# Kernel optimization log

Measured on AMD Instinct MI355X. Metric: run time of the kernel, lower is better.

The kernel has to match this reference:

```python
import jax, jax.numpy as jnp
import numpy as np

NF4 = jnp.array([-1.0, -0.6961928009986877, -0.5250730514526367, -0.39491748809814453,
                 -0.28444138169288635, -0.18477343022823334, -0.09105003625154495, 0.0,
                 0.07958029955625534, 0.16093020141124725, 0.24611230194568634,
                 0.33791524171829224, 0.44070982933044434, 0.5626170039176941,
                 0.7229568362236023, 1.0], dtype=jnp.float32)

IN_FEATURES = 2048
OUT_FEATURES = 8192
BLOCK_SIZE = 64


def setup_inputs() -> dict:
    key = jax.random.key(0)
    k1, k2, k3, k4 = jax.random.split(key, 4)
    n_elems = OUT_FEATURES * IN_FEATURES
    n_blocks = n_elems // BLOCK_SIZE
    x = jax.random.normal(k1, (2, 2048, IN_FEATURES), dtype=jnp.float32)
    q = jax.random.randint(k2, (n_elems,), 0, 16, dtype=jnp.int32)
    scale = jax.random.uniform(k3, (n_blocks,), dtype=jnp.float32)  # absmax >= 0
    bias = jax.random.normal(k4, (OUT_FEATURES,), dtype=jnp.float32)
    return {"x": x, "q": q, "scale": scale, "bias": bias}


def reference(x, q, scale, bias):
    # Dequantize: NF4 table lookup per 4-bit code, per-block absmax scale.
    n_blocks = scale.shape[0]
    codes = q.reshape(n_blocks, BLOCK_SIZE)                  # (n_blocks, 64)
    w = NF4[codes] * scale[:, None]                          # (n_blocks, 64)
    w = w.reshape(OUT_FEATURES, IN_FEATURES)                 # (out, in)
    # F.linear: y = x @ W^T + b
    return jnp.einsum('bsi,oi->bso', x, w) + bias
```

## Files before the change

### kernel.cpp

```cpp
#include <hip/hip_runtime.h>
#include <stdint.h>

#define GM 4096
#define GN 8192
#define GK 2048

typedef float f32x4 __attribute__((ext_vector_type(4)));
typedef __bf16 bf16x8 __attribute__((ext_vector_type(8)));

__device__ __constant__ float NF4_LUT[16] = {
    -1.0f, -0.6961928009986877f, -0.5250730514526367f, -0.39491748809814453f,
    -0.28444138169288635f, -0.18477343022823334f, -0.09105003625154495f, 0.0f,
    0.07958029955625534f, 0.16093020141124725f, 0.24611230194568634f,
    0.33791524171829224f, 0.44070982933044434f, 0.5626170039176941f,
    0.7229568362236023f, 1.0f};

__device__ __forceinline__ unsigned short f32_to_bf16_rne(float f) {
  union { float f; uint32_t u; } v;
  v.f = f;
  uint32_t lsb = (v.u >> 16) & 1u;
  v.u += 0x7fffu + lsb;
  return (unsigned short)(v.u >> 16);
}

__global__ void __launch_bounds__(256) dequant_nf4_kernel(
    const int* __restrict__ q, const float* __restrict__ scale,
    unsigned short* __restrict__ w) {
  __shared__ float lut[16];
  if (threadIdx.x < 16) lut[threadIdx.x] = NF4_LUT[threadIdx.x];
  __syncthreads();
  int t = blockIdx.x * 256 + threadIdx.x;
  const int4* q4 = reinterpret_cast<const int4*>(q);
  int4 c0 = q4[2 * t];
  int4 c1 = q4[2 * t + 1];
  float s = scale[t >> 3];
  int codes[8] = {c0.x, c0.y, c0.z, c0.w, c1.x, c1.y, c1.z, c1.w};
  union { unsigned short u[8]; int4 v; } r;
#pragma unroll
  for (int j = 0; j < 8; ++j)
    r.u[j] = f32_to_bf16_rne(lut[codes[j] & 15] * s);
  reinterpret_cast<int4*>(w)[t] = r.v;
}

__global__ void __launch_bounds__(256) cvt_f32_bf16_kernel(
    const float* __restrict__ x, unsigned short* __restrict__ xb) {
  int t = blockIdx.x * 256 + threadIdx.x;
  const float4* x4 = reinterpret_cast<const float4*>(x);
  float4 a = x4[2 * t];
  float4 b = x4[2 * t + 1];
  union { unsigned short u[8]; int4 v; } r;
  r.u[0] = f32_to_bf16_rne(a.x); r.u[1] = f32_to_bf16_rne(a.y);
  r.u[2] = f32_to_bf16_rne(a.z); r.u[3] = f32_to_bf16_rne(a.w);
  r.u[4] = f32_to_bf16_rne(b.x); r.u[5] = f32_to_bf16_rne(b.y);
  r.u[6] = f32_to_bf16_rne(b.z); r.u[7] = f32_to_bf16_rne(b.w);
  reinterpret_cast<int4*>(xb)[t] = r.v;
}

#define AS1(p) ((const __attribute__((address_space(1))) void*)(p))
#define AS3(p) ((__attribute__((address_space(3))) void*)(p))
#define VM6() asm volatile("s_waitcnt vmcnt(6)" ::: "memory")
#define FENCE() asm volatile("" ::: "memory")
#define BAR() do { FENCE(); __builtin_amdgcn_s_barrier(); FENCE(); } while (0)

__global__ void __launch_bounds__(512, 2) gemm_8phase_kernel(
    const unsigned short* __restrict__ A,
    const unsigned short* __restrict__ B,
    const float* __restrict__ bias, float* __restrict__ C) {
  constexpr int BK = 64, NT = GK / BK;
  __shared__ __align__(16) unsigned short As[2 * 256 * 64];
  __shared__ __align__(16) unsigned short Bs[2 * 256 * 64];

  int bid = blockIdx.x;
  int swz = (bid & 7) * 64 + (bid >> 3);
  int brow = (swz >> 5) * 256;
  int bcol = (swz & 31) * 256;

  int tid = threadIdx.x;
  int lane = tid & 63;
  int wave = tid >> 6;
  int wr = wave >> 2;
  int wc = wave & 3;
  int fr = lane & 15;
  int slot = lane >> 4;
  int swc = (slot << 4) ^ ((fr & 7) << 4);

  const unsigned short* Abase = A + (size_t)brow * GK;
  const unsigned short* Bbase = B + (size_t)bcol * GK;

  int arow = (wr * 64 + fr) * 128;
  int brw = (wc * 32 + fr) * 128;

  f32x4 acc[8][4] = {};
  bf16x8 a0[2][4][2], a1[2][4][2], b0[2][2][2], b1[2][2][2];

  auto ldA = [&](int buf, int qm, int m, int kk) -> bf16x8 {
    int off = buf * 32768 + qm * 16384 + m * 2048 + arow + (swc ^ (kk << 6));
    return *reinterpret_cast<const bf16x8*>((const char*)As + off);
  };
  auto ldB = [&](int buf, int qn, int n, int kk) -> bf16x8 {
    int off = buf * 32768 + qn * 16384 + n * 2048 + brw + (swc ^ (kk << 6));
    return *reinterpret_cast<const bf16x8*>((const char*)Bs + off);
  };
  auto stage = [&](const unsigned short* gtile, unsigned short* lds, int buf,
                   int h, int kt) {
#pragma unroll
    for (int i = 0; i < 2; ++i) {
      int L = h * 16384 + i * 8192 + tid * 16;
      int s = L ^ (((L >> 7) & 7) << 4);
      __builtin_amdgcn_global_load_lds(
          AS1(gtile + (size_t)(s >> 7) * GK + kt + ((s & 127) >> 1)),
          AS3((char*)lds + buf * 32768 + L), 16, 0, 0);
    }
  };
  auto RD_A1 = [&](int p) {
#pragma unroll
    for (int m = 0; m < 4; ++m)
#pragma unroll
      for (int kk = 0; kk < 2; ++kk) a1[p][m][kk] = ldA(p, 1, m, kk);
  };
  auto RD_B1 = [&](int p) {
#pragma unroll
    for (int n = 0; n < 2; ++n)
#pragma unroll
      for (int kk = 0; kk < 2; ++kk) b1[p][n][kk] = ldB(p, 1, n, kk);
  };
  auto RD_A0B0 = [&](int p) {
#pragma unroll
    for (int m = 0; m < 4; ++m)
#pragma unroll
      for (int kk = 0; kk < 2; ++kk) a0[p][m][kk] = ldA(p, 0, m, kk);
#pragma unroll
    for (int n = 0; n < 2; ++n)
#pragma unroll
      for (int kk = 0; kk < 2; ++kk) b0[p][n][kk] = ldB(p, 0, n, kk);
  };
  auto Q1 = [&](int p) {
    __builtin_amdgcn_s_setprio(1);
#pragma unroll
    for (int m = 0; m < 4; ++m)
#pragma unroll
      for (int n = 0; n < 2; ++n)
#pragma unroll
        for (int kk = 0; kk < 2; ++kk)
          acc[m][n] = __builtin_amdgcn_mfma_f32_16x16x32_bf16(
              a0[p][m][kk], b0[p][n][kk], acc[m][n], 0, 0, 0);
    __builtin_amdgcn_s_setprio(0);
  };
  auto Q2 = [&](int p) {
    __builtin_amdgcn_s_setprio(1);
#pragma unroll
    for (int m = 0; m < 4; ++m)
#pragma unroll
      for (int n = 0; n < 2; ++n)
#pragma unroll
        for (int kk = 0; kk < 2; ++kk)
          acc[4 + m][n] = __builtin_amdgcn_mfma_f32_16x16x32_bf16(
              a1[p][m][kk], b0[p][n][kk], acc[4 + m][n], 0, 0, 0);
    __builtin_amdgcn_s_setprio(0);
  };
  auto Q3 = [&](int p) {
    __builtin_amdgcn_s_setprio(1);
#pragma unroll
    for (int m = 0; m < 4; ++m)
#pragma unroll
      for (int n = 0; n < 2; ++n)
#pragma unroll
        for (int kk = 0; kk < 2; ++kk)
          acc[4 + m][2 + n] = __builtin_amdgcn_mfma_f32_16x16x32_bf16(
              a1[p][m][kk], b1[p][n][kk], acc[4 + m][2 + n], 0, 0, 0);
    __builtin_amdgcn_s_setprio(0);
  };
  auto Q4 = [&](int p) {
    __builtin_amdgcn_s_setprio(1);
#pragma unroll
    for (int m = 0; m < 4; ++m)
#pragma unroll
      for (int n = 0; n < 2; ++n)
#pragma unroll
        for (int kk = 0; kk < 2; ++kk)
          acc[m][2 + n] = __builtin_amdgcn_mfma_f32_16x16x32_bf16(
              a0[p][m][kk], b1[p][n][kk], acc[m][2 + n], 0, 0, 0);
    __builtin_amdgcn_s_setprio(0);
  };

  stage(Abase, As, 0, 0, 0);
  stage(Bbase, Bs, 0, 0, 0);
  stage(Abase, As, 0, 1, 0);
  stage(Bbase, Bs, 0, 1, 0);
  stage(Abase, As, 1, 0, BK);
  stage(Bbase, Bs, 1, 0, BK);
  stage(Abase, As, 1, 1, BK);
  VM6();
  BAR();
  RD_A0B0(0);

#pragma unroll 1
  for (int j = 0; j < NT / 2; ++j) {
    int t1 = 2 * j + 1;
    int t2 = (2 * j + 2 < NT) ? 2 * j + 2 : NT - 1;
    int t3 = (2 * j + 3 < NT) ? 2 * j + 3 : NT - 1;
    int kt1 = t1 * BK, kt2 = t2 * BK, kt3 = t3 * BK;
    RD_A1(0);
    stage(Bbase, Bs, 1, 1, kt1);
    BAR();
    Q1(0);
    RD_B1(0);
    BAR();
    Q2(0);
    stage(Abase, As, 0, 0, kt2);
    stage(Bbase, Bs, 0, 0, kt2);
    BAR();
    Q3(0);
    stage(Abase, As, 0, 1, kt2);
    VM6();
    BAR();
    RD_A0B0(1);
    Q4(0);
    RD_A1(1);
    stage(Bbase, Bs, 0, 1, kt2);
    BAR();
    Q1(1);
    RD_B1(1);
    BAR();
    Q2(1);
    stage(Abase, As, 1, 0, kt3);
    stage(Bbase, Bs, 1, 0, kt3);
    BAR();
    Q3(1);
    stage(Abase, As, 1, 1, kt3);
    VM6();
    BAR();
    RD_A0B0(0);
    Q4(1);
  }

  float bv[4];
#pragma unroll
  for (int n = 0; n < 4; ++n)
    bv[n] = bias[bcol + (n >> 1) * 128 + wc * 32 + (n & 1) * 16 + fr];
#pragma unroll
  for (int m = 0; m < 8; ++m) {
    int grow0 = brow + (m >> 2) * 128 + wr * 64 + (m & 3) * 16 + slot * 4;
#pragma unroll
    for (int n = 0; n < 4; ++n) {
      int gcol = bcol + (n >> 1) * 128 + wc * 32 + (n & 1) * 16 + fr;
#pragma unroll
      for (int r = 0; r < 4; ++r)
        C[(size_t)(grow0 + r) * GN + gcol] = acc[m][n][r] + bv[n];
    }
  }
}

__global__ void __launch_bounds__(256) fallback_kernel(
    const float* __restrict__ x, const int* __restrict__ q,
    const float* __restrict__ scale, const float* __restrict__ bias,
    float* __restrict__ out) {
  __shared__ float wrow[GK];
  int n = blockIdx.x;
  for (int k = threadIdx.x; k < GK; k += 256) {
    size_t idx = (size_t)n * GK + k;
    wrow[k] = NF4_LUT[q[idx] & 15] * scale[idx >> 6];
  }
  __syncthreads();
  int m = blockIdx.y * 256 + threadIdx.x;
  const float* xr = x + (size_t)m * GK;
  float acc = 0.f;
  for (int k = 0; k < GK; ++k) acc += xr[k] * wrow[k];
  out[(size_t)m * GN + n] = acc + bias[n];
}

extern "C" void kernel_launch(void* const* d_in, const int* in_sizes, int n_in,
                              void* d_out, int out_size, void* d_ws, size_t ws_size,
                              hipStream_t stream) {
  const float* x = (const float*)d_in[0];
  const int* q = (const int*)d_in[1];
  const float* scale = (const float*)d_in[2];
  const float* bias = (const float*)d_in[3];
  float* out = (float*)d_out;

  const size_t wbytes = (size_t)GN * GK * 2;
  const size_t xbytes = (size_t)GM * GK * 2;

  if (ws_size >= wbytes + xbytes) {
    unsigned short* wq = (unsigned short*)d_ws;
    unsigned short* xb = (unsigned short*)((char*)d_ws + wbytes);
    dequant_nf4_kernel<<<(GN * GK / 8) / 256, 256, 0, stream>>>(q, scale, wq);
    cvt_f32_bf16_kernel<<<(GM * GK / 8) / 256, 256, 0, stream>>>(x, xb);
    gemm_8phase_kernel<<<dim3((GM / 256) * (GN / 256)), 512, 0, stream>>>(
        xb, wq, bias, out);
  } else {
    fallback_kernel<<<dim3(GN, GM / 256), 256, 0, stream>>>(x, q, scale, bias, out);
  }
}
```

Before: 155.7 us.

## Make GEMM persistent over two N-tiles, chaining K-loops across tiles

Each workgroup now computes two adjacent 256x256 output tiles in sequence, treating them as one continuous 64-step K stream so prefetch of the second tile's data overlaps the first tile's tail. The grid shrinks to 256 workgroups, one per CU, and launch bounds change to one block per CU. The point is to remove per-tile prologue/epilogue pipeline bubbles and the wave-quantization tail of 512 tiles. The cost is lower occupancy and a mid-kernel output flush that stalls the loop.

```diff
diff --git a/kernel.cpp b/kernel.cpp
--- a/kernel.cpp
+++ b/kernel.cpp
@@ -62,18 +62,20 @@
 #define FENCE() asm volatile("" ::: "memory")
 #define BAR() do { FENCE(); __builtin_amdgcn_s_barrier(); FENCE(); } while (0)
 
-__global__ void __launch_bounds__(512, 2) gemm_8phase_kernel(
+__global__ void __launch_bounds__(512, 1) gemm_8phase_kernel(
     const unsigned short* __restrict__ A,
     const unsigned short* __restrict__ B,
     const float* __restrict__ bias, float* __restrict__ C) {
-  constexpr int BK = 64, NT = GK / BK;
+  constexpr int BK = 64;
+  constexpr int NV = 64;
   __shared__ __align__(16) unsigned short As[2 * 256 * 64];
   __shared__ __align__(16) unsigned short Bs[2 * 256 * 64];
 
   int bid = blockIdx.x;
-  int swz = (bid & 7) * 64 + (bid >> 3);
-  int brow = (swz >> 5) * 256;
-  int bcol = (swz & 31) * 256;
+  int swz = (bid & 7) * 32 + (bid >> 3);
+  int brow = (swz & 15) * 256;
+  int pair = swz >> 4;
+  int bcol0 = pair * 512;
 
   int tid = threadIdx.x;
   int lane = tid & 63;
@@ -85,7 +87,8 @@
   int swc = (slot << 4) ^ ((fr & 7) << 4);
 
   const unsigned short* Abase = A + (size_t)brow * GK;
-  const unsigned short* Bbase = B + (size_t)bcol * GK;
+  const unsigned short* Bbase0 = B + (size_t)bcol0 * GK;
+  const unsigned short* Bbase1 = Bbase0 + (size_t)256 * GK;
 
   int arow = (wr * 64 + fr) * 128;
   int brw = (wc * 32 + fr) * 128;
@@ -182,73 +185,90 @@
               a0[p][m][kk], b1[p][n][kk], acc[m][2 + n], 0, 0, 0);
     __builtin_amdgcn_s_setprio(0);
   };
+  auto flush = [&](int bc) {
+    float bv[4];
+#pragma unroll
+    for (int n = 0; n < 4; ++n)
+      bv[n] = bias[bc + (n >> 1) * 128 + wc * 32 + (n & 1) * 16 + fr];
+#pragma unroll
+    for (int m = 0; m < 8; ++m) {
+      int grow0 = brow + (m >> 2) * 128 + wr * 64 + (m & 3) * 16 + slot * 4;
+#pragma unroll
+      for (int n = 0; n < 4; ++n) {
+        int gcol = bc + (n >> 1) * 128 + wc * 32 + (n & 1) * 16 + fr;
+#pragma unroll
+        for (int r = 0; r < 4; ++r)
+          C[(size_t)(grow0 + r) * GN + gcol] = acc[m][n][r] + bv[n];
+      }
+    }
+  };
+  auto iter = [&](int j) {
+    int t1 = 2 * j + 1;
+    int t2 = 2 * j + 2; if (t2 > NV - 1) t2 = NV - 1;
+    int t3 = 2 * j + 3; if (t3 > NV - 1) t3 = NV - 1;
+    const unsigned short* B1p = (t1 < 32) ? Bbase0 : Bbase1;
+    const unsigned short* B2p = (t2 < 32) ? Bbase0 : Bbase1;
+    const unsigned short* B3p = (t3 < 32) ? Bbase0 : Bbase1;
+    int kt1 = (t1 & 31) * BK, kt2 = (t2 & 31) * BK, kt3 = (t3 & 31) * BK;
+    RD_A1(0);
+    stage(B1p, Bs, 1, 1, kt1);
+    BAR();
+    Q1(0);
+    RD_B1(0);
+    BAR();
+    Q2(0);
+    stage(Abase, As, 0, 0, kt2);
+    stage(B2p, Bs, 0, 0, kt2);
+    BAR();
+    Q3(0);
+    stage(Abase, As, 0, 1, kt2);
+    VM6();
+    BAR();
+    RD_A0B0(1);
+    Q4(0);
+    RD_A1(1);
+    stage(B2p, Bs, 0, 1, kt2);
+    BAR();
+    Q1(1);
+    RD_B1(1);
+    BAR();
+    Q2(1);
+    stage(Abase, As, 1, 0, kt3);
+    stage(B3p, Bs, 1, 0, kt3);
+    BAR();
+    Q3(1);
+    stage(Abase, As, 1, 1, kt3);
+    VM6();
+    BAR();
+    RD_A0B0(0);
+    Q4(1);
+  };
 
   stage(Abase, As, 0, 0, 0);
-  stage(Bbase, Bs, 0, 0, 0);
+  stage(Bbase0, Bs, 0, 0, 0);
   stage(Abase, As, 0, 1, 0);
-  stage(Bbase, Bs, 0, 1, 0);
+  stage(Bbase0, Bs, 0, 1, 0);
   stage(Abase, As, 1, 0, BK);
-  stage(Bbase, Bs, 1, 0, BK);
+  stage(Bbase0, Bs, 1, 0, BK);
   stage(Abase, As, 1, 1, BK);
   VM6();
   BAR();
   RD_A0B0(0);
 
 #pragma unroll 1
-  for (int j = 0; j < NT / 2; ++j) {
-    int t1 = 2 * j + 1;
-    int t2 = (2 * j + 2 < NT) ? 2 * j + 2 : NT - 1;
-    int t3 = (2 * j + 3 < NT) ? 2 * j + 3 : NT - 1;
-    int kt1 = t1 * BK, kt2 = t2 * BK, kt3 = t3 * BK;
-    RD_A1(0);
-    stage(Bbase, Bs, 1, 1, kt1);
-    BAR();
-    Q1(0);
-    RD_B1(0);
-    BAR();
-    Q2(0);
-    stage(Abase, As, 0, 0, kt2);
-    stage(Bbase, Bs, 0, 0, kt2);
-    BAR();
-    Q3(0);
-    stage(Abase, As, 0, 1, kt2);
-    VM6();
-    BAR();
-    RD_A0B0(1);
-    Q4(0);
-    RD_A1(1);
-    stage(Bbase, Bs, 0, 1, kt2);
-    BAR();
-    Q1(1);
-    RD_B1(1);
-    BAR();
-    Q2(1);
-    stage(Abase, As, 1, 0, kt3);
-    stage(Bbase, Bs, 1, 0, kt3);
-    BAR();
-    Q3(1);
-    stage(Abase, As, 1, 1, kt3);
-    VM6();
-    BAR();
-    RD_A0B0(0);
-    Q4(1);
-  }
-
-  float bv[4];
-#pragma unroll
-  for (int n = 0; n < 4; ++n)
-    bv[n] = bias[bcol + (n >> 1) * 128 + wc * 32 + (n & 1) * 16 + fr];
-#pragma unroll
-  for (int m = 0; m < 8; ++m) {
-    int grow0 = brow + (m >> 2) * 128 + wr * 64 + (m & 3) * 16 + slot * 4;
-#pragma unroll
-    for (int n = 0; n < 4; ++n) {
-      int gcol = bcol + (n >> 1) * 128 + wc * 32 + (n & 1) * 16 + fr;
-#pragma unroll
-      for (int r = 0; r < 4; ++r)
-        C[(size_t)(grow0 + r) * GN + gcol] = acc[m][n][r] + bv[n];
-    }
-  }
+  for (int j = 0; j < 16; ++j) iter(j);
+
+  flush(bcol0);
+#pragma unroll
+  for (int m = 0; m < 8; ++m)
+#pragma unroll
+    for (int n = 0; n < 4; ++n)
+      acc[m][n] = f32x4{0.f, 0.f, 0.f, 0.f};
+
+#pragma unroll 1
+  for (int j = 16; j < 32; ++j) iter(j);
+
+  flush(bcol0 + 256);
 }
 
 __global__ void __launch_bounds__(256) fallback_kernel(
@@ -286,8 +306,7 @@
     unsigned short* xb = (unsigned short*)((char*)d_ws + wbytes);
     dequant_nf4_kernel<<<(GN * GK / 8) / 256, 256, 0, stream>>>(q, scale, wq);
     cvt_f32_bf16_kernel<<<(GM * GK / 8) / 256, 256, 0, stream>>>(x, xb);
-    gemm_8phase_kernel<<<dim3((GM / 256) * (GN / 256)), 512, 0, stream>>>(
-        xb, wq, bias, out);
+    gemm_8phase_kernel<<<dim3(256), 512, 0, stream>>>(xb, wq, bias, out);
   } else {
     fallback_kernel<<<dim3(GN, GM / 256), 256, 0, stream>>>(x, q, scale, bias, out);
   }
```

After: 154.2 us. No clear change (-1.0%).
